# Kernel optimization log

Hardware: AMD Instinct MI355X
Metric: run time of the kernel (lower is better)

## Reference

```python
import jax, jax.numpy as jnp
import numpy as np

B, N = 8, 4096
NPOINT, RADIUS, NSAMPLE = 1024, 0.5, 32
IN_C = 64
MLP = [64, 64, 128]
EPS = 1e-5


def _gather(p, idx):
    # p: (B,N,C), idx: (B,...) int -> (B,...,C)
    return jax.vmap(lambda a, i: a[i])(p, idx)


def farthest_point_sample(xyz, npoint):
    b, n, _ = xyz.shape
    def step(carry, _):
        distance, farthest = carry
        centroid = _gather(xyz, farthest[:, None])              # (B,1,3)
        d = jnp.sum((xyz - centroid) ** 2, axis=-1)             # (B,N)
        distance = jnp.minimum(distance, d)
        nxt = jnp.argmax(distance, axis=-1).astype(jnp.int32)
        return (distance, nxt), farthest
    init = (jnp.full((b, n), 1e10, xyz.dtype), jnp.zeros((b,), jnp.int32))
    _, idx = jax.lax.scan(step, init, None, length=npoint)
    return idx.T                                                 # (B,npoint)


def query_ball_point(radius, nsample, xyz, new_xyz):
    b, n, _ = xyz.shape
    s = new_xyz.shape[1]
    sqr = jnp.sum((new_xyz[:, :, None, :] - xyz[:, None, :, :]) ** 2, axis=-1)  # (B,S,N)
    grp = jnp.broadcast_to(jnp.arange(n, dtype=jnp.int32), (b, s, n))
    grp = jnp.where(sqr > radius ** 2, n, grp)
    grp = jnp.sort(grp, axis=-1)[:, :, :nsample]                 # (B,S,K)
    first = grp[:, :, :1]
    return jnp.where(grp == n, first, grp)


def _sa_forward(xyz, points, params):
    fps_idx = farthest_point_sample(xyz, NPOINT)
    new_xyz = _gather(xyz, fps_idx)                              # (B,S,3)
    idx = query_ball_point(RADIUS, NSAMPLE, xyz, new_xyz)        # (B,S,K)
    grouped_xyz = _gather(xyz, idx)                              # (B,S,K,3)
    grouped_norm = grouped_xyz - new_xyz[:, :, None, :]
    grouped_pts = _gather(points, idx)                           # (B,S,K,C)
    feat = jnp.concatenate([grouped_xyz, grouped_norm, grouped_pts], axis=-1)
    for w, bias, gamma, beta in params:
        feat = jnp.einsum('bski,oi->bsko', feat, w) + bias       # 1x1 conv
        mean = feat.mean(axis=(0, 1, 2))                         # BN (train stats)
        var = feat.var(axis=(0, 1, 2))
        feat = (feat - mean) * jax.lax.rsqrt(var + EPS) * gamma + beta
        feat = jax.nn.relu(feat)
    new_points = feat.max(axis=2)                                # max over neighbors
    return new_xyz, new_points


def setup_inputs() -> dict:
    key = jax.random.key(0)
    ks = jax.random.split(key, 8)
    inp = {
        'xyz': jax.random.normal(ks[0], (B, N, 3), jnp.float32),
        'points': jax.random.normal(ks[1], (B, N, IN_C), jnp.float32),
    }
    last = IN_C + 6
    for li, out in enumerate(MLP):
        inp[f'w{li}'] = jax.random.normal(ks[2 + li], (out, last), jnp.float32) * 0.05
        inp[f'b{li}'] = jnp.zeros((out,), jnp.float32)
        inp[f'g{li}'] = jnp.ones((out,), jnp.float32)
        inp[f'be{li}'] = jnp.zeros((out,), jnp.float32)
        last = out
    return inp


def reference(xyz, points, w0, b0, g0, be0, w1, b1, g1, be1, w2, b2, g2, be2):
    params = [(w0, b0, g0, be0), (w1, b1, g1, be1), (w2, b2, g2, be2)]
    return _sa_forward(xyz, points, params)
```

## Files before the change

kernel.cpp:

```cpp
#include <hip/hip_runtime.h>

#define DI __device__ __forceinline__

#define B_ 8
#define N_ 4096
#define S_ 1024
#define K_ 32
#define M_TOT (B_ * S_ * K_)
#define NBLK 2048

DI float sqdist_rn(float ax, float ay, float az, float bx, float by, float bz) {
    float dx = __fsub_rn(ax, bx);
    float dy = __fsub_rn(ay, by);
    float dz = __fsub_rn(az, bz);
    return __fadd_rn(__fadd_rn(__fmul_rn(dx, dx), __fmul_rn(dy, dy)), __fmul_rn(dz, dz));
}

DI unsigned short f2b(float f) {
    unsigned u = __float_as_uint(f);
    return (unsigned short)((u + 0x7FFFu + ((u >> 16) & 1u)) >> 16);
}
DI float b2f(unsigned short h) { return __uint_as_float(((unsigned)h) << 16); }

template <int CTRL>
DI unsigned long long dpp_u64(unsigned long long v) {
    unsigned lo = (unsigned)__builtin_amdgcn_update_dpp(
        0, (int)(unsigned)v, CTRL, 0xF, 0xF, true);
    unsigned hi = (unsigned)__builtin_amdgcn_update_dpp(
        0, (int)(unsigned)(v >> 32), CTRL, 0xF, 0xF, true);
    return ((unsigned long long)hi << 32) | lo;
}
DI unsigned long long umax64(unsigned long long a, unsigned long long b) {
    return a > b ? a : b;
}

__global__ __launch_bounds__(512) void fps_kernel(const float* __restrict__ xyz,
                                                  float* __restrict__ new_xyz) {
    const int b = blockIdx.x;
    const int t = threadIdx.x;
    const float* X = xyz + (size_t)b * (N_ * 3);
    __shared__ float4 pts[N_];
    __shared__ __align__(16) unsigned long long part[2][8];
    float px[8], py[8], pz[8], dd[8];
#pragma unroll
    for (int j = 0; j < 8; ++j) {
        int p = t + 512 * j;
        float x = X[p * 3 + 0], y = X[p * 3 + 1], z = X[p * 3 + 2];
        px[j] = x; py[j] = y; pz[j] = z; dd[j] = 1e10f;
        pts[p] = make_float4(x, y, z, 0.0f);
    }
    if (t == 0) {
        new_xyz[(size_t)b * (S_ * 3) + 0] = px[0];
        new_xyz[(size_t)b * (S_ * 3) + 1] = py[0];
        new_xyz[(size_t)b * (S_ * 3) + 2] = pz[0];
    }
    __syncthreads();
    float4 cent = pts[0];
    for (int i = 1; i < S_; ++i) {
        unsigned long long k0[8];
#pragma unroll
        for (int j = 0; j < 8; ++j) {
            float d = sqdist_rn(px[j], py[j], pz[j], cent.x, cent.y, cent.z);
            dd[j] = fminf(dd[j], d);
            k0[j] = ((unsigned long long)__float_as_uint(dd[j]) << 32) |
                    (unsigned long long)(~(unsigned)(t + 512 * j));
        }
        k0[0] = umax64(k0[0], k0[1]);
        k0[2] = umax64(k0[2], k0[3]);
        k0[4] = umax64(k0[4], k0[5]);
        k0[6] = umax64(k0[6], k0[7]);
        k0[0] = umax64(k0[0], k0[2]);
        k0[4] = umax64(k0[4], k0[6]);
        unsigned long long key = umax64(k0[0], k0[4]);
        key = umax64(key, dpp_u64<0x111>(key));
        key = umax64(key, dpp_u64<0x112>(key));
        key = umax64(key, dpp_u64<0x114>(key));
        key = umax64(key, dpp_u64<0x118>(key));
        key = umax64(key, dpp_u64<0x142>(key));
        key = umax64(key, dpp_u64<0x143>(key));
        if ((t & 63) == 63) part[i & 1][t >> 6] = key;
        __syncthreads();
        ulonglong2 q0 = *(const ulonglong2*)&part[i & 1][0];
        ulonglong2 q1 = *(const ulonglong2*)&part[i & 1][2];
        ulonglong2 q2 = *(const ulonglong2*)&part[i & 1][4];
        ulonglong2 q3 = *(const ulonglong2*)&part[i & 1][6];
        unsigned long long ka = umax64(umax64(q0.x, q0.y), umax64(q1.x, q1.y));
        unsigned long long kb = umax64(umax64(q2.x, q2.y), umax64(q3.x, q3.y));
        unsigned long long k = umax64(ka, kb);
        unsigned gidx = ~(unsigned)(k & 0xFFFFFFFFull);
        cent = pts[gidx];
        if (t == 0) {
            size_t o3 = ((size_t)b * S_ + i) * 3;
            new_xyz[o3 + 0] = cent.x;
            new_xyz[o3 + 1] = cent.y;
            new_xyz[o3 + 2] = cent.z;
        }
    }
}

__global__ __launch_bounds__(256) void qb_kernel(const float* __restrict__ xyz,
                                                 const float* __restrict__ new_xyz,
                                                 int* __restrict__ idxbuf) {
    const int c = blockIdx.x * 4 + (threadIdx.x >> 6);
    const int lane = threadIdx.x & 63;
    const int b = c >> 10;
    const float* X = xyz + (size_t)b * (N_ * 3);
    const float cx = new_xyz[c * 3 + 0];
    const float cy = new_xyz[c * 3 + 1];
    const float cz = new_xyz[c * 3 + 2];
    int* out = idxbuf + (size_t)c * K_;
    int taken = 0, first = -1;
    for (int ch = 0; ch < 64; ++ch) {
        int p = ch * 64 + lane;
        float d = sqdist_rn(X[p * 3 + 0], X[p * 3 + 1], X[p * 3 + 2], cx, cy, cz);
        bool ok = (d <= 0.25f);
        unsigned long long m = __ballot(ok);
        if (first < 0 && m) first = ch * 64 + (__ffsll((unsigned long long)m) - 1);
        int pos = taken + (int)__popcll(m & ((1ull << lane) - 1ull));
        if (ok && pos < K_) out[pos] = p;
        taken += (int)__popcll(m);
        if (taken >= K_) break;
    }
    int filled = taken < K_ ? taken : K_;
    if (lane >= filled && lane < K_) out[lane] = first;
}

template <int FS, int SLOTS, int CC>
DI void gemm_tile(const float* __restrict__ feat, const float* __restrict__ wl,
                  const float* __restrict__ bias, unsigned short* __restrict__ yout,
                  float* __restrict__ ps, float* __restrict__ pq,
                  int r0, int tid, int blk) {
    const int tr = tid & 15;
    const int tc = tid >> 4;
    float acc[8][CC];
#pragma unroll
    for (int rr = 0; rr < 8; ++rr)
#pragma unroll
        for (int cc = 0; cc < CC; ++cc) acc[rr][cc] = 0.0f;

#pragma unroll 2
    for (int sl = 0; sl < SLOTS; ++sl) {
        float4 xv[8], wv[CC];
#pragma unroll
        for (int rr = 0; rr < 8; ++rr)
            xv[rr] = *(const float4*)&feat[(tr + 16 * rr) * FS + 4 * sl];
#pragma unroll
        for (int cc = 0; cc < CC; ++cc)
            wv[cc] = *(const float4*)&wl[(tc + 16 * cc) * FS + 4 * sl];
#pragma unroll
        for (int rr = 0; rr < 8; ++rr)
#pragma unroll
            for (int cc = 0; cc < CC; ++cc)
                acc[rr][cc] = fmaf(xv[rr].x, wv[cc].x,
                               fmaf(xv[rr].y, wv[cc].y,
                                fmaf(xv[rr].z, wv[cc].z,
                                 fmaf(xv[rr].w, wv[cc].w, acc[rr][cc]))));
    }
    float s1[CC], s2[CC];
#pragma unroll
    for (int cc = 0; cc < CC; ++cc) {
        const int och = tc + 16 * cc;
        const float bv = bias[och];
        s1[cc] = 0.0f; s2[cc] = 0.0f;
#pragma unroll
        for (int rr = 0; rr < 8; ++rr) {
            float y = acc[rr][cc] + bv;
            const int gr = r0 + tr + 16 * rr;
            yout[(size_t)gr * (16 * CC) + och] = f2b(y);
            s1[cc] += y;
            s2[cc] = fmaf(y, y, s2[cc]);
        }
    }
#pragma unroll
    for (int m = 1; m < 16; m <<= 1) {
#pragma unroll
        for (int cc = 0; cc < CC; ++cc) {
            s1[cc] += __shfl_xor(s1[cc], m);
            s2[cc] += __shfl_xor(s2[cc], m);
        }
    }
    if ((tid & 15) == 0) {
#pragma unroll
        for (int cc = 0; cc < CC; ++cc) {
            const int och = tc + 16 * cc;
            ps[och * NBLK + blk] = s1[cc];
            pq[och * NBLK + blk] = s2[cc];
        }
    }
}

__global__ __launch_bounds__(256) void layer1_kernel(
    const float* __restrict__ xyz, const float* __restrict__ points,
    const float* __restrict__ new_xyz, const int* __restrict__ idxbuf,
    const float* __restrict__ W, const float* __restrict__ bias,
    unsigned short* __restrict__ yout, float* __restrict__ ps, float* __restrict__ pq) {
    const int tid = threadIdx.x;
    const int blk = blockIdx.x;
    const int r0 = blk * 128;
    __shared__ float feat[128 * 76];
    __shared__ float wl[64 * 76];
    for (int jj = tid; jj < 64 * 70; jj += 256) {
        int o = jj / 70;
        int i = jj - o * 70;
        int mch = (i < 6) ? i : (i + 2);
        wl[o * 76 + mch] = W[jj];
    }
    if (tid < 128) wl[(tid >> 1) * 76 + 6 + (tid & 1)] = 0.0f;
    {
        const int row = tid >> 1, h = tid & 1;
        const int gr = r0 + row;
        const int b = gr >> 15;
        const int s = (gr >> 5) & 1023;
        const int pi = idxbuf[gr];
        const float* P = points + ((size_t)b * N_ + pi) * 64 + h * 32;
        float* fr = &feat[row * 76];
#pragma unroll
        for (int q = 0; q < 8; ++q) {
            float4 v = *(const float4*)(P + 4 * q);
            *(float4*)(fr + 8 + h * 32 + 4 * q) = v;
        }
        if (h == 0) {
            size_t pb = ((size_t)b * N_ + pi) * 3;
            float x = xyz[pb + 0], y = xyz[pb + 1], z = xyz[pb + 2];
            const float* C = new_xyz + ((size_t)b * S_ + s) * 3;
            fr[0] = x; fr[1] = y; fr[2] = z;
            fr[3] = x - C[0]; fr[4] = y - C[1]; fr[5] = z - C[2];
            fr[6] = 0.0f; fr[7] = 0.0f;
        }
    }
    __syncthreads();
    gemm_tile<76, 18, 4>(feat, wl, bias, yout, ps, pq, r0, tid, blk);
}

template <int OC>
__global__ __launch_bounds__(256) void layer23_kernel(
    const unsigned short* __restrict__ yin,
    const float* __restrict__ scale, const float* __restrict__ shift,
    const float* __restrict__ W, const float* __restrict__ bias,
    unsigned short* __restrict__ yout, float* __restrict__ ps, float* __restrict__ pq) {
    const int tid = threadIdx.x;
    const int blk = blockIdx.x;
    const int r0 = blk * 128;
    __shared__ float feat[128 * 68];
    __shared__ float wl[OC * 68];
    __shared__ float ssc[64], ssh[64];
    if (tid < 64) { ssc[tid] = scale[tid]; ssh[tid] = shift[tid]; }
    for (int jj = tid; jj < OC * 64; jj += 256) {
        int o = jj >> 6, i = jj & 63;
        wl[o * 68 + i] = W[jj];
    }
    __syncthreads();
    {
        const int row = tid >> 1, h = tid & 1;
        const int gr = r0 + row;
        const uint4* src = (const uint4*)(yin + (size_t)gr * 64 + h * 32);
        float* fr = &feat[row * 68 + h * 32];
#pragma unroll
        for (int q = 0; q < 4; ++q) {
            uint4 u = src[q];
            const int cb = h * 32 + q * 8;
            float f0 = fmaxf(fmaf(__uint_as_float(u.x << 16),         ssc[cb + 0], ssh[cb + 0]), 0.f);
            float f1 = fmaxf(fmaf(__uint_as_float(u.x & 0xFFFF0000u), ssc[cb + 1], ssh[cb + 1]), 0.f);
            float f2 = fmaxf(fmaf(__uint_as_float(u.y << 16),         ssc[cb + 2], ssh[cb + 2]), 0.f);
            float f3 = fmaxf(fmaf(__uint_as_float(u.y & 0xFFFF0000u), ssc[cb + 3], ssh[cb + 3]), 0.f);
            float f4 = fmaxf(fmaf(__uint_as_float(u.z << 16),         ssc[cb + 4], ssh[cb + 4]), 0.f);
            float f5 = fmaxf(fmaf(__uint_as_float(u.z & 0xFFFF0000u), ssc[cb + 5], ssh[cb + 5]), 0.f);
            float f6 = fmaxf(fmaf(__uint_as_float(u.w << 16),         ssc[cb + 6], ssh[cb + 6]), 0.f);
            float f7 = fmaxf(fmaf(__uint_as_float(u.w & 0xFFFF0000u), ssc[cb + 7], ssh[cb + 7]), 0.f);
            *(float4*)(fr + 8 * q)     = make_float4(f0, f1, f2, f3);
            *(float4*)(fr + 8 * q + 4) = make_float4(f4, f5, f6, f7);
        }
    }
    __syncthreads();
    gemm_tile<68, 16, OC / 16>(feat, wl, bias, yout, ps, pq, r0, tid, blk);
}

__global__ __launch_bounds__(256) void bn_reduce_kernel(
    const float* __restrict__ ps, const float* __restrict__ pq,
    const float* __restrict__ gamma, const float* __restrict__ beta,
    float* __restrict__ scale, float* __restrict__ shift) {
    const int o = blockIdx.x, t = threadIdx.x;
    float s1 = 0.f, s2 = 0.f;
    for (int i = t; i < NBLK; i += 256) {
        s1 += ps[o * NBLK + i];
        s2 += pq[o * NBLK + i];
    }
#pragma unroll
    for (int m = 32; m >= 1; m >>= 1) { s1 += __shfl_xor(s1, m); s2 += __shfl_xor(s2, m); }
    __shared__ float a1[4], a2[4];
    if ((t & 63) == 0) { a1[t >> 6] = s1; a2[t >> 6] = s2; }
    __syncthreads();
    if (t == 0) {
        float S1 = a1[0] + a1[1] + a1[2] + a1[3];
        float S2 = a2[0] + a2[1] + a2[2] + a2[3];
        const float inv = 1.0f / (float)M_TOT;
        float mean = S1 * inv;
        float var = S2 * inv - mean * mean;
        if (var < 0.f) var = 0.f;
        float rstd = 1.0f / sqrtf(var + 1e-5f);
        float sc = rstd * gamma[o];
        scale[o] = sc;
        shift[o] = beta[o] - mean * sc;
    }
}

__global__ __launch_bounds__(256) void pool_kernel(
    const unsigned short* __restrict__ y3,
    const float* __restrict__ scale, const float* __restrict__ shift,
    float* __restrict__ outp) {
    const int grp = blockIdx.x * 2 + (threadIdx.x >> 7);
    const int ch = threadIdx.x & 127;
    const unsigned short* Y = y3 + (size_t)grp * (K_ * 128) + ch;
    const float sc = scale[ch], sh = shift[ch];
    float m = -1e30f;
#pragma unroll 8
    for (int k = 0; k < K_; ++k) {
        float v = b2f(Y[k * 128]);
        m = fmaxf(m, fmaf(v, sc, sh));
    }
    outp[(size_t)grp * 128 + ch] = fmaxf(m, 0.0f);
}

extern "C" void kernel_launch(void* const* d_in, const int* in_sizes, int n_in,
                              void* d_out, int out_size, void* d_ws, size_t ws_size,
                              hipStream_t stream) {
    const float* xyz    = (const float*)d_in[0];
    const float* points = (const float*)d_in[1];
    const float* w0  = (const float*)d_in[2];
    const float* b0  = (const float*)d_in[3];
    const float* g0  = (const float*)d_in[4];
    const float* be0 = (const float*)d_in[5];
    const float* w1  = (const float*)d_in[6];
    const float* b1  = (const float*)d_in[7];
    const float* g1  = (const float*)d_in[8];
    const float* be1 = (const float*)d_in[9];
    const float* w2  = (const float*)d_in[10];
    const float* b2  = (const float*)d_in[11];
    const float* g2  = (const float*)d_in[12];
    const float* be2 = (const float*)d_in[13];

    float* out = (float*)d_out;
    char* ws = (char*)d_ws;
    int*   idxbuf = (int*)ws;
    float* ps  = (float*)(ws + (1 << 20));
    float* pq  = (float*)(ws + (2 << 20));
    float* st  = (float*)(ws + (3 << 20));
    float *sc0 = st,        *sh0 = st + 128;
    float *sc1 = st + 256,  *sh1 = st + 384;
    float *sc2 = st + 512,  *sh2 = st + 640;
    unsigned short* y1 = (unsigned short*)(ws + (4 << 20));
    unsigned short* y3 = y1;
    unsigned short* y2 = (unsigned short*)(ws + (68 << 20));

    fps_kernel<<<8, 512, 0, stream>>>(xyz, out);
    qb_kernel<<<2048, 256, 0, stream>>>(xyz, out, idxbuf);
    layer1_kernel<<<NBLK, 256, 0, stream>>>(xyz, points, out, idxbuf, w0, b0, y1, ps, pq);
    bn_reduce_kernel<<<64, 256, 0, stream>>>(ps, pq, g0, be0, sc0, sh0);
    layer23_kernel<64><<<NBLK, 256, 0, stream>>>(y1, sc0, sh0, w1, b1, y2, ps, pq);
    bn_reduce_kernel<<<64, 256, 0, stream>>>(ps, pq, g1, be1, sc1, sh1);
    layer23_kernel<128><<<NBLK, 256, 0, stream>>>(y2, sc1, sh1, w2, b2, y3, ps, pq);
    bn_reduce_kernel<<<128, 256, 0, stream>>>(ps, pq, g2, be2, sc2, sh2);
    pool_kernel<<<4096, 256, 0, stream>>>(y3, sc2, sh2, out + 24576);
}
```

Baseline: 968.9 us.

## Use bf16 MFMA for layers 2-3 and fuse max/min pooling into layer 3

Layers 2 and 3 now run on bf16 MFMA (16x16x32) over swizzled LDS tiles of 256 rows, replacing the scalar fp32 gemm_tile. Layer 3 no longer writes its full activation. It records per-group max and min of the pre-BN output, so the final pooling only applies the affine transform to max and min, which stays correct for negative scales. Inputs and weights are rounded to bf16 before the matmul, which may change precision slightly.

```diff
diff --git a/kernel.cpp b/kernel.cpp
--- a/kernel.cpp
+++ b/kernel.cpp
@@ -8,6 +8,10 @@
 #define K_ 32
 #define M_TOT (B_ * S_ * K_)
 #define NBLK 2048
+#define NW 4096
+
+typedef short bf16x8 __attribute__((ext_vector_type(8)));
+typedef float f32x4 __attribute__((ext_vector_type(4)));
 
 DI float sqdist_rn(float ax, float ay, float az, float bx, float by, float bz) {
     float dx = __fsub_rn(ax, bx);
@@ -232,58 +236,141 @@
     gemm_tile<76, 18, 4>(feat, wl, bias, yout, ps, pq, r0, tid, blk);
 }
 
-template <int OC>
-__global__ __launch_bounds__(256) void layer23_kernel(
+template <int OC, bool LAST>
+__global__ __launch_bounds__(256) void layerM_kernel(
     const unsigned short* __restrict__ yin,
     const float* __restrict__ scale, const float* __restrict__ shift,
     const float* __restrict__ W, const float* __restrict__ bias,
-    unsigned short* __restrict__ yout, float* __restrict__ ps, float* __restrict__ pq) {
+    unsigned short* __restrict__ yout,
+    float* __restrict__ ps, float* __restrict__ pq,
+    float* __restrict__ maxb, float* __restrict__ minb) {
     const int tid = threadIdx.x;
     const int blk = blockIdx.x;
-    const int r0 = blk * 128;
-    __shared__ float feat[128 * 68];
-    __shared__ float wl[OC * 68];
+    const int r0 = blk * 256;
+    __shared__ unsigned short featA[256 * 64];
+    __shared__ unsigned short wlT[OC * 64];
     __shared__ float ssc[64], ssh[64];
     if (tid < 64) { ssc[tid] = scale[tid]; ssh[tid] = shift[tid]; }
-    for (int jj = tid; jj < OC * 64; jj += 256) {
-        int o = jj >> 6, i = jj & 63;
-        wl[o * 68 + i] = W[jj];
+#pragma unroll
+    for (int it = 0; it < OC / 16; ++it) {
+        int q = it * 256 + tid;
+        int och = q >> 4;
+        int qq = q & 15;
+        float4 wv = *(const float4*)&W[q * 4];
+        uint2 pk;
+        pk.x = (unsigned)f2b(wv.x) | ((unsigned)f2b(wv.y) << 16);
+        pk.y = (unsigned)f2b(wv.z) | ((unsigned)f2b(wv.w) << 16);
+        int idx = och * 64 + (((qq * 8) ^ ((och & 7) << 4)) >> 1);
+        *(uint2*)&wlT[idx] = pk;
     }
     __syncthreads();
-    {
-        const int row = tid >> 1, h = tid & 1;
-        const int gr = r0 + row;
-        const uint4* src = (const uint4*)(yin + (size_t)gr * 64 + h * 32);
-        float* fr = &feat[row * 68 + h * 32];
-#pragma unroll
-        for (int q = 0; q < 4; ++q) {
-            uint4 u = src[q];
-            const int cb = h * 32 + q * 8;
-            float f0 = fmaxf(fmaf(__uint_as_float(u.x << 16),         ssc[cb + 0], ssh[cb + 0]), 0.f);
-            float f1 = fmaxf(fmaf(__uint_as_float(u.x & 0xFFFF0000u), ssc[cb + 1], ssh[cb + 1]), 0.f);
-            float f2 = fmaxf(fmaf(__uint_as_float(u.y << 16),         ssc[cb + 2], ssh[cb + 2]), 0.f);
-            float f3 = fmaxf(fmaf(__uint_as_float(u.y & 0xFFFF0000u), ssc[cb + 3], ssh[cb + 3]), 0.f);
-            float f4 = fmaxf(fmaf(__uint_as_float(u.z << 16),         ssc[cb + 4], ssh[cb + 4]), 0.f);
-            float f5 = fmaxf(fmaf(__uint_as_float(u.z & 0xFFFF0000u), ssc[cb + 5], ssh[cb + 5]), 0.f);
-            float f6 = fmaxf(fmaf(__uint_as_float(u.w << 16),         ssc[cb + 6], ssh[cb + 6]), 0.f);
-            float f7 = fmaxf(fmaf(__uint_as_float(u.w & 0xFFFF0000u), ssc[cb + 7], ssh[cb + 7]), 0.f);
-            *(float4*)(fr + 8 * q)     = make_float4(f0, f1, f2, f3);
-            *(float4*)(fr + 8 * q + 4) = make_float4(f4, f5, f6, f7);
-        }
+#pragma unroll
+    for (int it = 0; it < 8; ++it) {
+        int f = it * 256 + tid;
+        int row = f >> 3, g = f & 7;
+        uint4 u = *(const uint4*)&yin[(size_t)(r0 + row) * 64 + g * 8];
+        int c = g * 8;
+        float f0 = fmaxf(fmaf(__uint_as_float(u.x << 16),         ssc[c + 0], ssh[c + 0]), 0.f);
+        float f1 = fmaxf(fmaf(__uint_as_float(u.x & 0xFFFF0000u), ssc[c + 1], ssh[c + 1]), 0.f);
+        float f2 = fmaxf(fmaf(__uint_as_float(u.y << 16),         ssc[c + 2], ssh[c + 2]), 0.f);
+        float f3 = fmaxf(fmaf(__uint_as_float(u.y & 0xFFFF0000u), ssc[c + 3], ssh[c + 3]), 0.f);
+        float f4 = fmaxf(fmaf(__uint_as_float(u.z << 16),         ssc[c + 4], ssh[c + 4]), 0.f);
+        float f5 = fmaxf(fmaf(__uint_as_float(u.z & 0xFFFF0000u), ssc[c + 5], ssh[c + 5]), 0.f);
+        float f6 = fmaxf(fmaf(__uint_as_float(u.w << 16),         ssc[c + 6], ssh[c + 6]), 0.f);
+        float f7 = fmaxf(fmaf(__uint_as_float(u.w & 0xFFFF0000u), ssc[c + 7], ssh[c + 7]), 0.f);
+        uint4 pk;
+        pk.x = (unsigned)f2b(f0) | ((unsigned)f2b(f1) << 16);
+        pk.y = (unsigned)f2b(f2) | ((unsigned)f2b(f3) << 16);
+        pk.z = (unsigned)f2b(f4) | ((unsigned)f2b(f5) << 16);
+        pk.w = (unsigned)f2b(f6) | ((unsigned)f2b(f7) << 16);
+        int idx = row * 64 + (((g * 16) ^ ((row & 7) << 4)) >> 1);
+        *(uint4*)&featA[idx] = pk;
     }
     __syncthreads();
-    gemm_tile<68, 16, OC / 16>(feat, wl, bias, yout, ps, pq, r0, tid, blk);
-}
-
+    const int w = tid >> 6, l = tid & 63;
+    const int lr = l & 15, lg = l >> 4;
+    const int wrow0 = w * 64;
+    f32x4 acc[4][OC / 16];
+#pragma unroll
+    for (int mf = 0; mf < 4; ++mf)
+#pragma unroll
+        for (int nf = 0; nf < OC / 16; ++nf)
+#pragma unroll
+            for (int r = 0; r < 4; ++r) acc[mf][nf][r] = 0.0f;
+#pragma unroll
+    for (int kc = 0; kc < 2; ++kc) {
+        const int kb = kc * 64 + lg * 16;
+        bf16x8 bfr[OC / 16];
+#pragma unroll
+        for (int nf = 0; nf < OC / 16; ++nf) {
+            int och = nf * 16 + lr;
+            bfr[nf] = *(const bf16x8*)&wlT[och * 64 + ((kb ^ ((och & 7) << 4)) >> 1)];
+        }
+#pragma unroll
+        for (int mf = 0; mf < 4; ++mf) {
+            int row = wrow0 + mf * 16 + lr;
+            bf16x8 af = *(const bf16x8*)&featA[row * 64 + ((kb ^ ((row & 7) << 4)) >> 1)];
+#pragma unroll
+            for (int nf = 0; nf < OC / 16; ++nf)
+                acc[mf][nf] = __builtin_amdgcn_mfma_f32_16x16x32_bf16(
+                    af, bfr[nf], acc[mf][nf], 0, 0, 0);
+        }
+    }
+    const int gwave = blk * 4 + w;
+#pragma unroll
+    for (int nf = 0; nf < OC / 16; ++nf) {
+        const int och = nf * 16 + lr;
+        const float bv = bias[och];
+        float s1 = 0.f, s2 = 0.f;
+        float mx0 = -1e30f, mn0 = 1e30f, mx1 = -1e30f, mn1 = 1e30f;
+#pragma unroll
+        for (int mf = 0; mf < 4; ++mf) {
+#pragma unroll
+            for (int r = 0; r < 4; ++r) {
+                float y = acc[mf][nf][r] + bv;
+                s1 += y;
+                s2 = fmaf(y, y, s2);
+                if (LAST) {
+                    if (mf < 2) { mx0 = fmaxf(mx0, y); mn0 = fminf(mn0, y); }
+                    else        { mx1 = fmaxf(mx1, y); mn1 = fminf(mn1, y); }
+                } else {
+                    int gr = r0 + wrow0 + mf * 16 + lg * 4 + r;
+                    yout[(size_t)gr * OC + och] = f2b(y);
+                }
+            }
+        }
+        s1 += __shfl_xor(s1, 16); s1 += __shfl_xor(s1, 32);
+        s2 += __shfl_xor(s2, 16); s2 += __shfl_xor(s2, 32);
+        if (LAST) {
+            mx0 = fmaxf(mx0, __shfl_xor(mx0, 16)); mx0 = fmaxf(mx0, __shfl_xor(mx0, 32));
+            mn0 = fminf(mn0, __shfl_xor(mn0, 16)); mn0 = fminf(mn0, __shfl_xor(mn0, 32));
+            mx1 = fmaxf(mx1, __shfl_xor(mx1, 16)); mx1 = fmaxf(mx1, __shfl_xor(mx1, 32));
+            mn1 = fminf(mn1, __shfl_xor(mn1, 16)); mn1 = fminf(mn1, __shfl_xor(mn1, 32));
+        }
+        if (l < 16) {
+            ps[och * NW + gwave] = s1;
+            pq[och * NW + gwave] = s2;
+            if (LAST) {
+                int grp0 = blk * 8 + w * 2;
+                maxb[(size_t)grp0 * OC + och] = mx0;
+                minb[(size_t)grp0 * OC + och] = mn0;
+                maxb[(size_t)(grp0 + 1) * OC + och] = mx1;
+                minb[(size_t)(grp0 + 1) * OC + och] = mn1;
+            }
+        }
+    }
+}
+
+template <int NPART>
 __global__ __launch_bounds__(256) void bn_reduce_kernel(
     const float* __restrict__ ps, const float* __restrict__ pq,
     const float* __restrict__ gamma, const float* __restrict__ beta,
     float* __restrict__ scale, float* __restrict__ shift) {
     const int o = blockIdx.x, t = threadIdx.x;
     float s1 = 0.f, s2 = 0.f;
-    for (int i = t; i < NBLK; i += 256) {
-        s1 += ps[o * NBLK + i];
-        s2 += pq[o * NBLK + i];
+    for (int i = t; i < NPART; i += 256) {
+        s1 += ps[o * NPART + i];
+        s2 += pq[o * NPART + i];
     }
 #pragma unroll
     for (int m = 32; m >= 1; m >>= 1) { s1 += __shfl_xor(s1, m); s2 += __shfl_xor(s2, m); }
@@ -304,21 +391,16 @@
     }
 }
 
-__global__ __launch_bounds__(256) void pool_kernel(
-    const unsigned short* __restrict__ y3,
+__global__ __launch_bounds__(256) void pool2_kernel(
+    const float* __restrict__ maxb, const float* __restrict__ minb,
     const float* __restrict__ scale, const float* __restrict__ shift,
     float* __restrict__ outp) {
-    const int grp = blockIdx.x * 2 + (threadIdx.x >> 7);
-    const int ch = threadIdx.x & 127;
-    const unsigned short* Y = y3 + (size_t)grp * (K_ * 128) + ch;
-    const float sc = scale[ch], sh = shift[ch];
-    float m = -1e30f;
-#pragma unroll 8
-    for (int k = 0; k < K_; ++k) {
-        float v = b2f(Y[k * 128]);
-        m = fmaxf(m, fmaf(v, sc, sh));
-    }
-    outp[(size_t)grp * 128 + ch] = fmaxf(m, 0.0f);
+    int idx = blockIdx.x * 256 + threadIdx.x;
+    int och = idx & 127;
+    float sc = scale[och], sh = shift[och];
+    float a = fmaf(maxb[idx], sc, sh);
+    float b = fmaf(minb[idx], sc, sh);
+    outp[idx] = fmaxf(fmaxf(a, b), 0.0f);
 }
 
 extern "C" void kernel_launch(void* const* d_in, const int* in_sizes, int n_in,
@@ -343,22 +425,25 @@
     char* ws = (char*)d_ws;
     int*   idxbuf = (int*)ws;
     float* ps  = (float*)(ws + (1 << 20));
-    float* pq  = (float*)(ws + (2 << 20));
-    float* st  = (float*)(ws + (3 << 20));
+    float* pq  = (float*)(ws + (3 << 20));
+    float* st  = (float*)(ws + (5 << 20));
     float *sc0 = st,        *sh0 = st + 128;
     float *sc1 = st + 256,  *sh1 = st + 384;
     float *sc2 = st + 512,  *sh2 = st + 640;
-    unsigned short* y1 = (unsigned short*)(ws + (4 << 20));
-    unsigned short* y3 = y1;
-    unsigned short* y2 = (unsigned short*)(ws + (68 << 20));
+    float* maxb = (float*)(ws + (6 << 20));
+    float* minb = (float*)(ws + (10 << 20));
+    unsigned short* y1 = (unsigned short*)(ws + (14 << 20));
+    unsigned short* y2 = (unsigned short*)(ws + (46 << 20));
 
     fps_kernel<<<8, 512, 0, stream>>>(xyz, out);
     qb_kernel<<<2048, 256, 0, stream>>>(xyz, out, idxbuf);
     layer1_kernel<<<NBLK, 256, 0, stream>>>(xyz, points, out, idxbuf, w0, b0, y1, ps, pq);
-    bn_reduce_kernel<<<64, 256, 0, stream>>>(ps, pq, g0, be0, sc0, sh0);
-    layer23_kernel<64><<<NBLK, 256, 0, stream>>>(y1, sc0, sh0, w1, b1, y2, ps, pq);
-    bn_reduce_kernel<<<64, 256, 0, stream>>>(ps, pq, g1, be1, sc1, sh1);
-    layer23_kernel<128><<<NBLK, 256, 0, stream>>>(y2, sc1, sh1, w2, b2, y3, ps, pq);
-    bn_reduce_kernel<<<128, 256, 0, stream>>>(ps, pq, g2, be2, sc2, sh2);
-    pool_kernel<<<4096, 256, 0, stream>>>(y3, sc2, sh2, out + 24576);
-}
+    bn_reduce_kernel<NBLK><<<64, 256, 0, stream>>>(ps, pq, g0, be0, sc0, sh0);
+    layerM_kernel<64, false><<<M_TOT / 256, 256, 0, stream>>>(
+        y1, sc0, sh0, w1, b1, y2, ps, pq, nullptr, nullptr);
+    bn_reduce_kernel<NW><<<64, 256, 0, stream>>>(ps, pq, g1, be1, sc1, sh1);
+    layerM_kernel<128, true><<<M_TOT / 256, 256, 0, stream>>>(
+        y2, sc1, sh1, w2, b2, nullptr, ps, pq, maxb, minb);
+    bn_reduce_kernel<NW><<<128, 256, 0, stream>>>(ps, pq, g2, be2, sc2, sh2);
+    pool2_kernel<<<4096, 256, 0, stream>>>(maxb, minb, sc2, sh2, out + 24576);
+}
```

After: 853.3 us. 1.14x faster.
